# Kernel optimization log

Hardware: AMD Instinct MI355X
Metric: run time of the kernel (lower is better)

The kernel has to match this reference:

```python
import jax, jax.numpy as jnp
import numpy as np

NUM_EMBEDDINGS = 16384
EMBED_DIM = 256
COMMITMENT_COST = 0.25  # legacy=True: vq_loss = commit + beta * codebook


def setup_inputs() -> dict:
    key = jax.random.key(0)
    k1, k2, k3, k4 = jax.random.split(key, 4)
    z = jax.random.normal(k1, (8, 2048, EMBED_DIM), dtype=jnp.float32)
    # frozen codebook: normal(0, embedding_dim ** -0.5)
    codebook = jax.random.normal(k2, (NUM_EMBEDDINGS, EMBED_DIM), dtype=jnp.float32) * (EMBED_DIM ** -0.5)
    # learnable linear projection, torch default uniform init
    bound = 1.0 / np.sqrt(EMBED_DIM)
    proj_w = jax.random.uniform(k3, (EMBED_DIM, EMBED_DIM), dtype=jnp.float32, minval=-bound, maxval=bound)
    proj_b = jax.random.uniform(k4, (EMBED_DIM,), dtype=jnp.float32, minval=-bound, maxval=bound)
    return {"z": z, "codebook": codebook, "proj_w": proj_w, "proj_b": proj_b}


def reference(z, codebook, proj_w, proj_b):
    B, T, D = z.shape
    # projected codebook (the only learned part of the quantizer)
    quant_codebook = codebook @ proj_w.T + proj_b  # [K, D]
    z_flat = z.reshape(-1, D)  # [N, D]
    # squared L2 distances: ||z||^2 + ||c||^2 - 2 z.c
    dists = (
        jnp.sum(z_flat * z_flat, axis=1, keepdims=True)
        + jnp.sum(quant_codebook * quant_codebook, axis=1)
        - 2.0 * jnp.einsum("nd,kd->nk", z_flat, quant_codebook)
    )  # [N, K]
    idx = jnp.argmin(dists, axis=1)  # [N]
    quantized = quant_codebook[idx].reshape(z.shape)  # [B, T, D]

    commitment_loss = jnp.mean((jax.lax.stop_gradient(quantized) - z) ** 2)
    codebook_loss = jnp.mean((quantized - jax.lax.stop_gradient(z)) ** 2)
    vq_loss = commitment_loss + COMMITMENT_COST * codebook_loss  # legacy formulation

    # straight-through estimator
    quantized = z + jax.lax.stop_gradient(quantized - z)
    encoding_indices = idx.reshape(B, T)
    return quantized, vq_loss, encoding_indices
```

## Files before the change

kernel.cpp:

```cpp
#include <hip/hip_runtime.h>

typedef unsigned short u16;
typedef __bf16 bf16x8 __attribute__((ext_vector_type(8)));
typedef float f32x4 __attribute__((ext_vector_type(4)));

#define NQ 16384
#define NC 16384
#define DD 256
#define BM 128
#define BN 128
#define BK 64
#define NSPLIT 8
#define NPART (NSPLIT * 2)
#define NTILES ((NC / NSPLIT) / BN)

__device__ __forceinline__ u16 f2bf(float x) {
  unsigned u = __float_as_uint(x);
  u += 0x7fffu + ((u >> 16) & 1u);
  return (u16)(u >> 16);
}
__device__ __forceinline__ float bf2f(u16 h) {
  return __uint_as_float(((unsigned)h) << 16);
}

__device__ __forceinline__ void gl2lds16(const void* g, void* l) {
  __builtin_amdgcn_global_load_lds((__attribute__((address_space(1))) void*)g,
                                   (__attribute__((address_space(3))) void*)l,
                                   16, 0, 0);
}

__global__ __launch_bounds__(256) void split_z_kernel(const float* __restrict__ z,
                                                      u16* __restrict__ Ah,
                                                      u16* __restrict__ Al) {
  size_t i = (size_t)blockIdx.x * 256 + threadIdx.x;
  float4 v = ((const float4*)z)[i];
  float f[4] = {v.x, v.y, v.z, v.w};
  u16 hh[4], ll[4];
#pragma unroll
  for (int j = 0; j < 4; ++j) {
    hh[j] = f2bf(f[j]);
    ll[j] = f2bf(f[j] - bf2f(hh[j]));
  }
  ushort4 h; h.x = hh[0]; h.y = hh[1]; h.z = hh[2]; h.w = hh[3];
  ushort4 l; l.x = ll[0]; l.y = ll[1]; l.z = ll[2]; l.w = ll[3];
  ((ushort4*)Ah)[i] = h;
  ((ushort4*)Al)[i] = l;
}

__global__ __launch_bounds__(256) void norm256_kernel(const float* __restrict__ x,
                                                      float* __restrict__ nrm) {
  const int t = threadIdx.x;
  const int j = t & 7;
  const int row = blockIdx.x * 32 + (t >> 3);
  const float* q = x + (size_t)row * 256;
  float half[2];
#pragma unroll
  for (int h = 0; h < 2; ++h) {
    const float* p = q + h * 128;
    float v0 = p[j];
    float r = __fmul_rn(v0, v0);
#pragma unroll
    for (int i = 8; i < 128; i += 8) {
      float v = p[i + j];
      r = __fadd_rn(r, __fmul_rn(v, v));
    }
    float s1 = __fadd_rn(r, __shfl_xor(r, 1));
    float s2 = __fadd_rn(s1, __shfl_xor(s1, 2));
    half[h] = __fadd_rn(s2, __shfl_xor(s2, 4));
  }
  if (j == 0) nrm[row] = __fadd_rn(half[0], half[1]);
}

__global__ __launch_bounds__(256) void qc_gemm_kernel(const float* __restrict__ cb,
                                                      const float* __restrict__ W,
                                                      const float* __restrict__ bias,
                                                      float* __restrict__ qc) {
  __shared__ float As[64][33];
  __shared__ float Bs[64][33];
  const int bm = blockIdx.x >> 2;
  const int bn = blockIdx.x & 3;
  const int m0 = bm * 64, n0 = bn * 64;
  const int t = threadIdx.x;
  const int tx = t & 15, ty = t >> 4;
  float acc[4][4] = {};
  for (int kc = 0; kc < 256; kc += 32) {
    __syncthreads();
#pragma unroll
    for (int j = 0; j < 8; ++j) {
      int idx = j * 256 + t;
      int r = idx >> 5, c = idx & 31;
      As[r][c] = cb[(size_t)(m0 + r) * 256 + kc + c];
      Bs[r][c] = W[(size_t)(n0 + r) * 256 + kc + c];
    }
    __syncthreads();
#pragma unroll
    for (int kk = 0; kk < 32; ++kk) {
      float a[4], b[4];
#pragma unroll
      for (int u = 0; u < 4; ++u) a[u] = As[ty * 4 + u][kk];
#pragma unroll
      for (int v = 0; v < 4; ++v) b[v] = Bs[tx * 4 + v][kk];
#pragma unroll
      for (int u = 0; u < 4; ++u)
#pragma unroll
        for (int v = 0; v < 4; ++v) acc[u][v] += a[u] * b[v];
    }
  }
#pragma unroll
  for (int u = 0; u < 4; ++u)
#pragma unroll
    for (int v = 0; v < 4; ++v) {
      int r = m0 + ty * 4 + u, c = n0 + tx * 4 + v;
      qc[(size_t)r * 256 + c] = acc[u][v] + bias[c];
    }
}

__global__ __launch_bounds__(256) void split_qc_kernel(const float* __restrict__ qc,
                                                       u16* __restrict__ Bh,
                                                       u16* __restrict__ Bl) {
  size_t i = (size_t)blockIdx.x * 256 + threadIdx.x;
  float4 v = ((const float4*)qc)[i];
  float f[4] = {v.x, v.y, v.z, v.w};
  u16 hh[4], ll[4];
#pragma unroll
  for (int j = 0; j < 4; ++j) {
    hh[j] = f2bf(f[j]);
    ll[j] = f2bf(f[j] - bf2f(hh[j]));
  }
  ushort4 h; h.x = hh[0]; h.y = hh[1]; h.z = hh[2]; h.w = hh[3];
  ushort4 l; l.x = ll[0]; l.y = ll[1]; l.z = ll[2]; l.w = ll[3];
  ((ushort4*)Bh)[i] = h;
  ((ushort4*)Bl)[i] = l;
}

__global__ __launch_bounds__(256, 2) void vq_argmin_kernel(
    const u16* __restrict__ Ah, const u16* __restrict__ Al,
    const u16* __restrict__ Bh, const u16* __restrict__ Bl,
    const float* __restrict__ cnorm, const float* __restrict__ znorm,
    float* __restrict__ pval, int* __restrict__ pidx) {
  __shared__ __align__(16) u16 Ahs[BM * BK];
  __shared__ __align__(16) u16 Als[BM * BK];
  __shared__ __align__(16) u16 Bhs[BN * BK];
  __shared__ __align__(16) u16 Bls[BN * BK];

  const int bm = blockIdx.x / NSPLIT;
  const int spl = blockIdx.x % NSPLIT;
  const int lane = threadIdx.x & 63;
  const int wid = threadIdx.x >> 6;
  const int wm = wid >> 1, wn = wid & 1;
  const int l15 = lane & 15;
  const int lg = lane >> 4;
  const int m0 = bm * BM;
  const int ns0 = spl * (NC / NSPLIT);

  const int st_r = lane >> 3;
  const int st_g = (((lane & 7) ^ (lane >> 3)) << 3);

  float zrow[4][4];
#pragma unroll
  for (int mi = 0; mi < 4; ++mi)
#pragma unroll
    for (int i = 0; i < 4; ++i)
      zrow[mi][i] = znorm[m0 + wm * 64 + mi * 16 + lg * 4 + i];

  float rmin[4][4];
  int ridx[4][4];
#pragma unroll
  for (int a = 0; a < 4; ++a)
#pragma unroll
    for (int b = 0; b < 4; ++b) { rmin[a][b] = 3.4e38f; ridx[a][b] = 0; }

  for (int nt = 0; nt < NTILES; ++nt) {
    const int n0 = ns0 + nt * BN;
    f32x4 acc[4][4];
#pragma unroll
    for (int a = 0; a < 4; ++a)
#pragma unroll
      for (int b = 0; b < 4; ++b) {
        f32x4 zz = {0.f, 0.f, 0.f, 0.f};
        acc[a][b] = zz;
      }

    for (int kc = 0; kc < DD; kc += BK) {
      __syncthreads();
#pragma unroll
      for (int j = 0; j < 4; ++j) {
        const int grp = wid * 4 + j;
        const int o = grp * 512;
        const int r = grp * 8 + st_r;
        const size_t ga = (size_t)(m0 + r) * DD + kc + st_g;
        const size_t gb = (size_t)(n0 + r) * DD + kc + st_g;
        gl2lds16(Ah + ga, Ahs + o);
        gl2lds16(Al + ga, Als + o);
        gl2lds16(Bh + gb, Bhs + o);
        gl2lds16(Bl + gb, Bls + o);
      }
      __syncthreads();
#pragma unroll
      for (int ks = 0; ks < BK; ks += 32) {
        const int c = (ks >> 3) + lg;
        bf16x8 ah[4], al[4], bh[4], bl[4];
#pragma unroll
        for (int mi = 0; mi < 4; ++mi) {
          const int r = wm * 64 + mi * 16 + l15;
          const int off = r * BK + ((c ^ (r & 7)) << 3);
          ah[mi] = *(const bf16x8*)&Ahs[off];
          al[mi] = *(const bf16x8*)&Als[off];
        }
#pragma unroll
        for (int ni = 0; ni < 4; ++ni) {
          const int r = wn * 64 + ni * 16 + l15;
          const int off = r * BK + ((c ^ (r & 7)) << 3);
          bh[ni] = *(const bf16x8*)&Bhs[off];
          bl[ni] = *(const bf16x8*)&Bls[off];
        }
#pragma unroll
        for (int mi = 0; mi < 4; ++mi)
#pragma unroll
          for (int ni = 0; ni < 4; ++ni) {
            acc[mi][ni] = __builtin_amdgcn_mfma_f32_16x16x32_bf16(ah[mi], bh[ni], acc[mi][ni], 0, 0, 0);
            acc[mi][ni] = __builtin_amdgcn_mfma_f32_16x16x32_bf16(ah[mi], bl[ni], acc[mi][ni], 0, 0, 0);
            acc[mi][ni] = __builtin_amdgcn_mfma_f32_16x16x32_bf16(al[mi], bh[ni], acc[mi][ni], 0, 0, 0);
          }
      }
    }
#pragma unroll
    for (int ni = 0; ni < 4; ++ni) {
      const int col = n0 + wn * 64 + ni * 16 + l15;
      const float cn = cnorm[col];
#pragma unroll
      for (int mi = 0; mi < 4; ++mi)
#pragma unroll
        for (int i = 0; i < 4; ++i) {
          const float s = __fadd_rn(zrow[mi][i], cn);
          const float v = __fsub_rn(s, __fmul_rn(2.0f, acc[mi][ni][i]));
          if (v < rmin[mi][i]) { rmin[mi][i] = v; ridx[mi][i] = col; }
        }
    }
  }
#pragma unroll
  for (int mi = 0; mi < 4; ++mi)
#pragma unroll
    for (int i = 0; i < 4; ++i) {
      float v = rmin[mi][i];
      int ix = ridx[mi][i];
#pragma unroll
      for (int d = 1; d < 16; d <<= 1) {
        float ov = __shfl_xor(v, d);
        int oi = __shfl_xor(ix, d);
        if (ov < v || (ov == v && oi < ix)) { v = ov; ix = oi; }
      }
      if (l15 == 0) {
        const int row = m0 + wm * 64 + mi * 16 + lg * 4 + i;
        const int part = spl * 2 + wn;
        pval[(size_t)part * NQ + row] = v;
        pidx[(size_t)part * NQ + row] = ix;
      }
    }
}

__global__ __launch_bounds__(256) void finalize_kernel(
    const float* __restrict__ pval, const int* __restrict__ pidx,
    const float* __restrict__ qc, const float* __restrict__ z,
    float* __restrict__ out, float* __restrict__ loss_acc) {
  __shared__ int sidx[8];
  __shared__ float red[256];
  const int bid = blockIdx.x;
  const int t = threadIdx.x;
  if (t < 8) {
    const int row = bid * 8 + t;
    float best = pval[row];
    int bi = pidx[row];
    for (int s2 = 1; s2 < NPART; ++s2) {
      float v = pval[(size_t)s2 * NQ + row];
      int ix = pidx[(size_t)s2 * NQ + row];
      if (v < best || (v == best && ix < bi)) { best = v; bi = ix; }
    }
    sidx[t] = bi;
    out[4194305 + row] = (float)bi;
  }
  __syncthreads();
  float d2 = 0.f;
#pragma unroll
  for (int r = 0; r < 8; ++r) {
    const int row = bid * 8 + r;
    const int ix = sidx[r];
    const float q = qc[(size_t)ix * 256 + t];
    const float zz = z[(size_t)row * 256 + t];
    out[(size_t)row * 256 + t] = q;
    const float d = q - zz;
    d2 += d * d;
  }
  red[t] = d2;
  for (int st = 128; st; st >>= 1) {
    __syncthreads();
    if (t < st) red[t] += red[t + st];
  }
  if (t == 0) atomicAdd(loss_acc, red[0]);
}

__global__ void write_loss_kernel(const float* __restrict__ loss_acc, float* __restrict__ out) {
  out[4194304] = 1.25f * loss_acc[0] / 4194304.0f;
}

extern "C" void kernel_launch(void* const* d_in, const int* in_sizes, int n_in,
                              void* d_out, int out_size, void* d_ws, size_t ws_size,
                              hipStream_t stream) {
  const float* z = (const float*)d_in[0];
  const float* cb = (const float*)d_in[1];
  const float* W = (const float*)d_in[2];
  const float* bias = (const float*)d_in[3];
  float* out = (float*)d_out;
  char* ws = (char*)d_ws;

  constexpr size_t OFF_QC = 0;
  constexpr size_t OFF_AH = OFF_QC + 16777216;
  constexpr size_t OFF_AL = OFF_AH + 8388608;
  constexpr size_t OFF_BH = OFF_AL + 8388608;
  constexpr size_t OFF_BL = OFF_BH + 8388608;
  constexpr size_t OFF_CN = OFF_BL + 8388608;
  constexpr size_t OFF_ZN = OFF_CN + 65536;
  constexpr size_t OFF_PV = OFF_ZN + 65536;
  constexpr size_t OFF_PI = OFF_PV + 1048576;
  constexpr size_t OFF_ACC = OFF_PI + 1048576;

  float* qc = (float*)(ws + OFF_QC);
  u16* Ah = (u16*)(ws + OFF_AH);
  u16* Al = (u16*)(ws + OFF_AL);
  u16* Bh = (u16*)(ws + OFF_BH);
  u16* Bl = (u16*)(ws + OFF_BL);
  float* cn = (float*)(ws + OFF_CN);
  float* zn = (float*)(ws + OFF_ZN);
  float* pv = (float*)(ws + OFF_PV);
  int* pi = (int*)(ws + OFF_PI);
  float* lacc = (float*)(ws + OFF_ACC);

  hipMemsetAsync(lacc, 0, 4, stream);
  split_z_kernel<<<4096, 256, 0, stream>>>(z, Ah, Al);
  qc_gemm_kernel<<<1024, 256, 0, stream>>>(cb, W, bias, qc);
  norm256_kernel<<<NQ / 32, 256, 0, stream>>>(z, zn);
  norm256_kernel<<<NC / 32, 256, 0, stream>>>(qc, cn);
  split_qc_kernel<<<4096, 256, 0, stream>>>(qc, Bh, Bl);
  vq_argmin_kernel<<<(NQ / BM) * NSPLIT, 256, 0, stream>>>(Ah, Al, Bh, Bl, cn, zn, pv, pi);
  finalize_kernel<<<NQ / 8, 256, 0, stream>>>(pv, pi, qc, z, out, lacc);
  write_loss_kernel<<<1, 1, 0, stream>>>(lacc, out);
}
```

Measured before the change: 551.5 us.

## Fuse prep kernels: z split with norm, qc GEMM with bf16 split

Merges the z bf16 hi/lo split with the z norm computation through a shared-memory staging buffer, and folds the qc bf16 split plus the loss-accumulator reset into the codebook projection GEMM. The GEMM moves to 128x128 tiles with 8x8 register blocking, transposed LDS tiles and float4 reads. The finalize gather is vectorised to float4. This removes the memset and two launches along with redundant global round trips. The cost is that the GEMM launches only 256 blocks with higher register pressure, and the prep stages are small next to the main argmin kernel.

After: 533.2 us. 1.03x faster.

```diff
diff --git a/kernel.cpp b/kernel.cpp
--- a/kernel.cpp
+++ b/kernel.cpp
@@ -29,22 +29,51 @@
                                    16, 0, 0);
 }
 
-__global__ __launch_bounds__(256) void split_z_kernel(const float* __restrict__ z,
-                                                      u16* __restrict__ Ah,
-                                                      u16* __restrict__ Al) {
-  size_t i = (size_t)blockIdx.x * 256 + threadIdx.x;
-  float4 v = ((const float4*)z)[i];
-  float f[4] = {v.x, v.y, v.z, v.w};
-  u16 hh[4], ll[4];
-#pragma unroll
-  for (int j = 0; j < 4; ++j) {
-    hh[j] = f2bf(f[j]);
-    ll[j] = f2bf(f[j] - bf2f(hh[j]));
-  }
-  ushort4 h; h.x = hh[0]; h.y = hh[1]; h.z = hh[2]; h.w = hh[3];
-  ushort4 l; l.x = ll[0]; l.y = ll[1]; l.z = ll[2]; l.w = ll[3];
-  ((ushort4*)Ah)[i] = h;
-  ((ushort4*)Al)[i] = l;
+__global__ __launch_bounds__(256) void split_z_norm_kernel(const float* __restrict__ z,
+                                                           u16* __restrict__ Ah,
+                                                           u16* __restrict__ Al,
+                                                           float* __restrict__ zn) {
+  __shared__ float zs[32 * 256];
+  const int t = threadIdx.x;
+#pragma unroll
+  for (int j = 0; j < 8; ++j) {
+    const int loc = j * 256 + t;
+    const size_t i = (size_t)blockIdx.x * 2048 + loc;
+    float4 v = ((const float4*)z)[i];
+    *(float4*)&zs[loc * 4] = v;
+    float f[4] = {v.x, v.y, v.z, v.w};
+    u16 hh[4], ll[4];
+#pragma unroll
+    for (int q = 0; q < 4; ++q) {
+      hh[q] = f2bf(f[q]);
+      ll[q] = f2bf(f[q] - bf2f(hh[q]));
+    }
+    ushort4 h; h.x = hh[0]; h.y = hh[1]; h.z = hh[2]; h.w = hh[3];
+    ushort4 l; l.x = ll[0]; l.y = ll[1]; l.z = ll[2]; l.w = ll[3];
+    ((ushort4*)Ah)[i] = h;
+    ((ushort4*)Al)[i] = l;
+  }
+  __syncthreads();
+  const int j = t & 7;
+  const int lrow = t >> 3;
+  const int row = blockIdx.x * 32 + lrow;
+  const float* q = zs + lrow * 256;
+  float half[2];
+#pragma unroll
+  for (int h = 0; h < 2; ++h) {
+    const float* p = q + h * 128;
+    float v0 = p[j];
+    float r = __fmul_rn(v0, v0);
+#pragma unroll
+    for (int i = 8; i < 128; i += 8) {
+      float v = p[i + j];
+      r = __fadd_rn(r, __fmul_rn(v, v));
+    }
+    float s1 = __fadd_rn(r, __shfl_xor(r, 1));
+    float s2 = __fadd_rn(s1, __shfl_xor(s1, 2));
+    half[h] = __fadd_rn(s2, __shfl_xor(s2, 4));
+  }
+  if (j == 0) zn[row] = __fadd_rn(half[0], half[1]);
 }
 
 __global__ __launch_bounds__(256) void norm256_kernel(const float* __restrict__ x,
@@ -74,63 +103,66 @@
 __global__ __launch_bounds__(256) void qc_gemm_kernel(const float* __restrict__ cb,
                                                       const float* __restrict__ W,
                                                       const float* __restrict__ bias,
-                                                      float* __restrict__ qc) {
-  __shared__ float As[64][33];
-  __shared__ float Bs[64][33];
-  const int bm = blockIdx.x >> 2;
-  const int bn = blockIdx.x & 3;
-  const int m0 = bm * 64, n0 = bn * 64;
+                                                      float* __restrict__ qc,
+                                                      u16* __restrict__ Bh,
+                                                      u16* __restrict__ Bl,
+                                                      float* __restrict__ loss_acc) {
+  __shared__ float At[32][132];
+  __shared__ float Bt[32][132];
+  if (blockIdx.x == 0 && threadIdx.x == 0) *loss_acc = 0.f;
+  const int bm = blockIdx.x >> 1;
+  const int bn = blockIdx.x & 1;
+  const int m0 = bm * 128, n0 = bn * 128;
   const int t = threadIdx.x;
   const int tx = t & 15, ty = t >> 4;
-  float acc[4][4] = {};
+  float acc[8][8] = {};
   for (int kc = 0; kc < 256; kc += 32) {
     __syncthreads();
 #pragma unroll
-    for (int j = 0; j < 8; ++j) {
-      int idx = j * 256 + t;
-      int r = idx >> 5, c = idx & 31;
-      As[r][c] = cb[(size_t)(m0 + r) * 256 + kc + c];
-      Bs[r][c] = W[(size_t)(n0 + r) * 256 + kc + c];
+    for (int j = 0; j < 16; ++j) {
+      const int idx = j * 256 + t;
+      const int r = idx >> 5, c = idx & 31;
+      At[c][r] = cb[(size_t)(m0 + r) * 256 + kc + c];
+      Bt[c][r] = W[(size_t)(n0 + r) * 256 + kc + c];
     }
     __syncthreads();
 #pragma unroll
     for (int kk = 0; kk < 32; ++kk) {
-      float a[4], b[4];
-#pragma unroll
-      for (int u = 0; u < 4; ++u) a[u] = As[ty * 4 + u][kk];
-#pragma unroll
-      for (int v = 0; v < 4; ++v) b[v] = Bs[tx * 4 + v][kk];
-#pragma unroll
-      for (int u = 0; u < 4; ++u)
-#pragma unroll
-        for (int v = 0; v < 4; ++v) acc[u][v] += a[u] * b[v];
-    }
-  }
-#pragma unroll
-  for (int u = 0; u < 4; ++u)
-#pragma unroll
-    for (int v = 0; v < 4; ++v) {
-      int r = m0 + ty * 4 + u, c = n0 + tx * 4 + v;
-      qc[(size_t)r * 256 + c] = acc[u][v] + bias[c];
-    }
-}
-
-__global__ __launch_bounds__(256) void split_qc_kernel(const float* __restrict__ qc,
-                                                       u16* __restrict__ Bh,
-                                                       u16* __restrict__ Bl) {
-  size_t i = (size_t)blockIdx.x * 256 + threadIdx.x;
-  float4 v = ((const float4*)qc)[i];
-  float f[4] = {v.x, v.y, v.z, v.w};
-  u16 hh[4], ll[4];
-#pragma unroll
-  for (int j = 0; j < 4; ++j) {
-    hh[j] = f2bf(f[j]);
-    ll[j] = f2bf(f[j] - bf2f(hh[j]));
-  }
-  ushort4 h; h.x = hh[0]; h.y = hh[1]; h.z = hh[2]; h.w = hh[3];
-  ushort4 l; l.x = ll[0]; l.y = ll[1]; l.z = ll[2]; l.w = ll[3];
-  ((ushort4*)Bh)[i] = h;
-  ((ushort4*)Bl)[i] = l;
+      float4 a0 = *(const float4*)&At[kk][ty * 8];
+      float4 a1 = *(const float4*)&At[kk][ty * 8 + 4];
+      float4 b0 = *(const float4*)&Bt[kk][tx * 8];
+      float4 b1 = *(const float4*)&Bt[kk][tx * 8 + 4];
+      float a[8] = {a0.x, a0.y, a0.z, a0.w, a1.x, a1.y, a1.z, a1.w};
+      float b[8] = {b0.x, b0.y, b0.z, b0.w, b1.x, b1.y, b1.z, b1.w};
+#pragma unroll
+      for (int u = 0; u < 8; ++u)
+#pragma unroll
+        for (int v = 0; v < 8; ++v) acc[u][v] += a[u] * b[v];
+    }
+  }
+#pragma unroll
+  for (int u = 0; u < 8; ++u) {
+    const int r = m0 + ty * 8 + u;
+#pragma unroll
+    for (int g = 0; g < 2; ++g) {
+      const int c0 = n0 + tx * 8 + g * 4;
+      float q4[4];
+#pragma unroll
+      for (int v = 0; v < 4; ++v) q4[v] = acc[u][g * 4 + v] + bias[c0 + v];
+      float4 qv; qv.x = q4[0]; qv.y = q4[1]; qv.z = q4[2]; qv.w = q4[3];
+      *(float4*)&qc[(size_t)r * 256 + c0] = qv;
+      u16 hh[4], ll[4];
+#pragma unroll
+      for (int v = 0; v < 4; ++v) {
+        hh[v] = f2bf(q4[v]);
+        ll[v] = f2bf(q4[v] - bf2f(hh[v]));
+      }
+      ushort4 h; h.x = hh[0]; h.y = hh[1]; h.z = hh[2]; h.w = hh[3];
+      ushort4 l; l.x = ll[0]; l.y = ll[1]; l.z = ll[2]; l.w = ll[3];
+      *(ushort4*)&Bh[(size_t)r * 256 + c0] = h;
+      *(ushort4*)&Bl[(size_t)r * 256 + c0] = l;
+    }
+  }
 }
 
 __global__ __launch_bounds__(256, 2) void vq_argmin_kernel(
@@ -280,16 +312,22 @@
     out[4194305 + row] = (float)bi;
   }
   __syncthreads();
+  const int r = t >> 5;
+  const int c0 = (t & 31) * 8;
+  const int row = bid * 8 + r;
+  const int ix = sidx[r];
+  const float4 q0 = *(const float4*)&qc[(size_t)ix * 256 + c0];
+  const float4 q1 = *(const float4*)&qc[(size_t)ix * 256 + c0 + 4];
+  const float4 z0 = *(const float4*)&z[(size_t)row * 256 + c0];
+  const float4 z1 = *(const float4*)&z[(size_t)row * 256 + c0 + 4];
+  *(float4*)&out[(size_t)row * 256 + c0] = q0;
+  *(float4*)&out[(size_t)row * 256 + c0 + 4] = q1;
   float d2 = 0.f;
-#pragma unroll
-  for (int r = 0; r < 8; ++r) {
-    const int row = bid * 8 + r;
-    const int ix = sidx[r];
-    const float q = qc[(size_t)ix * 256 + t];
-    const float zz = z[(size_t)row * 256 + t];
-    out[(size_t)row * 256 + t] = q;
-    const float d = q - zz;
-    d2 += d * d;
+  {
+    const float dq[8] = {q0.x - z0.x, q0.y - z0.y, q0.z - z0.z, q0.w - z0.w,
+                         q1.x - z1.x, q1.y - z1.y, q1.z - z1.z, q1.w - z1.w};
+#pragma unroll
+    for (int k = 0; k < 8; ++k) d2 += dq[k] * dq[k];
   }
   red[t] = d2;
   for (int st = 128; st; st >>= 1) {
@@ -335,12 +373,9 @@
   int* pi = (int*)(ws + OFF_PI);
   float* lacc = (float*)(ws + OFF_ACC);
 
-  hipMemsetAsync(lacc, 0, 4, stream);
-  split_z_kernel<<<4096, 256, 0, stream>>>(z, Ah, Al);
-  qc_gemm_kernel<<<1024, 256, 0, stream>>>(cb, W, bias, qc);
-  norm256_kernel<<<NQ / 32, 256, 0, stream>>>(z, zn);
+  split_z_norm_kernel<<<NQ / 32, 256, 0, stream>>>(z, Ah, Al, zn);
+  qc_gemm_kernel<<<256, 256, 0, stream>>>(cb, W, bias, qc, Bh, Bl, lacc);
   norm256_kernel<<<NC / 32, 256, 0, stream>>>(qc, cn);
-  split_qc_kernel<<<4096, 256, 0, stream>>>(qc, Bh, Bl);
   vq_argmin_kernel<<<(NQ / BM) * NSPLIT, 256, 0, stream>>>(Ah, Al, Bh, Bl, cn, zn, pv, pi);
   finalize_kernel<<<NQ / 8, 256, 0, stream>>>(pv, pi, qc, z, out, lacc);
   write_loss_kernel<<<1, 1, 0, stream>>>(lacc, out);
```
